# Kernel optimization log

Hardware: AMD Instinct MI355X
Metric: run time of the kernel (lower is better)

Reference implementation:

```python
import jax, jax.numpy as jnp
import numpy as np

B, T_H, N, F_P = 16, 24, 256, 6
H, PRED_LEN, F_W = 64, 12, 4


def _build_static(coords):
    # haversine distance matrix -> gaussian kernel -> threshold (epsilon=0.5)
    lon, lat = coords[:, 0], coords[:, 1]
    dlon = lon[None, :] - lon[:, None]
    dlat = lat[None, :] - lat[:, None]
    a = (np.sin(np.radians(dlat / 2)) ** 2
         + np.cos(np.radians(lat[:, None])) * np.cos(np.radians(lat[None, :]))
         * np.sin(np.radians(dlon / 2)) ** 2)
    dist = 2.0 * 6371.0 * np.arcsin(np.sqrt(np.clip(a, 0.0, None)))
    std = dist.flatten().std()
    adj = np.exp(-np.square(dist / std))
    adj[adj < 0.5] = 0.0
    return adj.astype(np.float32)


def setup_inputs() -> dict:
    key = jax.random.key(0)
    ks = jax.random.split(key, 16)
    rng = np.random.default_rng(0)
    coords_np = np.stack([116.0 + rng.uniform(-1.0, 1.0, N),
                          40.0 + rng.uniform(-1.0, 1.0, N)], axis=1).astype(np.float32)
    s = 0.05
    scale_w = jnp.asarray([1.0, 360.0, 10.0, 1.0], jnp.float32)  # [_, dir(deg), speed, _]
    return {
        "history_pollution": jax.random.normal(ks[0], (B, T_H, N, F_P), jnp.float32),
        "history_weather": jax.random.uniform(ks[1], (B, T_H, F_W), jnp.float32) * scale_w,
        "static_adj": jnp.asarray(_build_static(coords_np)),
        "coords": jnp.asarray(coords_np),
        "w_gc1": jax.random.normal(ks[2], (H, F_P), jnp.float32) * s,
        "b_gc1": jax.random.normal(ks[3], (H,), jnp.float32) * s,
        "w_gc2": jax.random.normal(ks[4], (H, H), jnp.float32) * s,
        "b_gc2": jax.random.normal(ks[5], (H,), jnp.float32) * s,
        "w_ih": jax.random.normal(ks[6], (3 * H, H), jnp.float32) * s,
        "w_hh": jax.random.normal(ks[7], (3 * H, H), jnp.float32) * s,
        "b_ih": jax.random.normal(ks[8], (3 * H,), jnp.float32) * s,
        "b_hh": jax.random.normal(ks[9], (3 * H,), jnp.float32) * s,
        "w_m1": jax.random.normal(ks[10], (32, H), jnp.float32) * s,
        "b_m1": jax.random.normal(ks[11], (32,), jnp.float32) * s,
        "w_m2": jax.random.normal(ks[12], (F_P, 32), jnp.float32) * s,
        "b_m2": jax.random.normal(ks[13], (F_P,), jnp.float32) * s,
    }


def _forward(history_pollution, history_weather, static_adj, coords,
             w_gc1, b_gc1, w_gc2, b_gc2, w_ih, w_hh, b_ih, b_hh,
             w_m1, b_m1, w_m2, b_m2):
    Bs, Th, Ns, Fp = history_pollution.shape
    dt = history_pollution.dtype
    eye = jnp.eye(Ns, dtype=dt)
    # station pair angles: vecs[i,j] = coords[j] - coords[i]
    vecs = coords[None, :, :] - coords[:, None, :]
    ang = jnp.arctan2(vecs[..., 1], vecs[..., 0])  # [N,N]

    def gconv(x, adj, w, b):
        wt = adj + eye[None]                         # [B,N,N]
        d = 1.0 / (jnp.sqrt(wt.sum(-1)) + 1e-6)      # [B,N]
        norm = d[:, :, None] * wt * d[:, None, :]    # D^-1/2 W D^-1/2
        return jnp.einsum('bij,bjf->bif', norm, x) @ w.T + b

    def gcb(x, w_out, w_in):
        h1 = jax.nn.relu(gconv(x, w_out, w_gc1, b_gc1))
        return jax.nn.relu(gconv(h1, w_in, w_gc2, b_gc2))

    def gru(h, x):                                   # h,x: [B*N,H]
        gi = x @ w_ih.T + b_ih
        gh = h @ w_hh.T + b_hh
        i_r, i_z, i_n = jnp.split(gi, 3, axis=-1)
        h_r, h_z, h_n = jnp.split(gh, 3, axis=-1)
        r = jax.nn.sigmoid(i_r + h_r)
        z = jax.nn.sigmoid(i_z + h_z)
        n = jnp.tanh(i_n + r * h_n)
        return (1.0 - z) * n + z * h

    def mlp(x):
        return jax.nn.relu(x @ w_m1.T + b_m1) @ w_m2.T + b_m2

    def enc_step(carry, xs):
        h, _ = carry
        x_t, spd, wd = xs                            # [B,N,F],[B],[B]
        rad = jnp.deg2rad(wd)
        w_dyn = jnp.maximum(spd[:, None, None] * jnp.cos(ang[None] - rad[:, None, None]), 0.0)
        w_out = static_adj[None] * w_dyn             # [B,N,N]
        sf = gcb(x_t, w_out, jnp.swapaxes(w_out, 1, 2))
        h = gru(h, sf.reshape(Bs * Ns, -1))
        return (h, w_out), None

    h0 = jnp.zeros((Bs * Ns, w_hh.shape[1]), dt)
    xs = (jnp.moveaxis(history_pollution, 1, 0),      # [T,B,N,F]
          history_weather[:, :, 2].T,                 # wind speed [T,B]
          history_weather[:, :, 1].T)                 # wind dir   [T,B]
    (h, last_w_out), _ = jax.lax.scan(enc_step, (h0, jnp.zeros((Bs, Ns, Ns), dt)), xs)
    last_w_in = jnp.swapaxes(last_w_out, 1, 2)

    dec0 = mlp(h.reshape(Bs, Ns, -1))

    def dec_step(carry, _):
        h_c, x = carry
        sf = gcb(x, last_w_out, last_w_in)
        h_c = gru(h_c, sf.reshape(Bs * Ns, -1))
        pred = mlp(h_c.reshape(Bs, Ns, -1))
        return (h_c, pred), pred

    _, preds = jax.lax.scan(dec_step, (h, dec0), None, length=PRED_LEN)
    return jnp.moveaxis(preds, 0, 1)                  # [B, pred_len, N, F_P]


def reference(history_pollution, history_weather, static_adj, coords,
              w_gc1, b_gc1, w_gc2, b_gc2, w_ih, w_hh, b_ih, b_hh,
              w_m1, b_m1, w_m2, b_m2):
    return _forward(history_pollution, history_weather, static_adj, coords,
                    w_gc1, b_gc1, w_gc2, b_gc2, w_ih, w_hh, b_ih, b_hh,
                    w_m1, b_m1, w_m2, b_m2)
```

## Files before the change

### kernel.cpp

```cpp
#include <hip/hip_runtime.h>
#include <math.h>

#define Bsz 16
#define Tt 24
#define Nn 256
#define Fp 6
#define Hh 64
#define PredL 12
#define Fw 4
#define M1 32
#define TCHUNK 12
#define DEG2RAD 0.017453292519943295f
#define IDX2(t, b) ((t) * Bsz + (b))

__global__ __launch_bounds__(256) void k_prep(
    const float* __restrict__ coords, const float* __restrict__ adj,
    const float* __restrict__ wgc2, const float* __restrict__ wih,
    const float* __restrict__ whh,  const float* __restrict__ wm1,
    const float* __restrict__ wm2,
    float2* __restrict__ pk,
    float* __restrict__ wgc2T, float* __restrict__ wm1T, float* __restrict__ wm2T,
    float4* __restrict__ wihP, float4* __restrict__ whhP) {
  int tid = threadIdx.x;
  if (blockIdx.x < Nn) {
    int i = blockIdx.x;
    int j = tid;
    float dx = coords[2 * j]     - coords[2 * i];
    float dy = coords[2 * j + 1] - coords[2 * i + 1];
    float ang = atan2f(dy, dx);
    float a = adj[i * Nn + j];
    pk[i * Nn + j] = make_float2(a * cosf(ang), a * sinf(ang));
    return;
  }
  for (int idx = tid; idx < Hh * Hh; idx += 256) {
    int g = idx / Hh, k = idx % Hh;
    wgc2T[k * Hh + g] = wgc2[g * Hh + k];
  }
  for (int idx = tid; idx < M1 * Hh; idx += 256) {
    int m = idx / Hh, k = idx % Hh;
    wm1T[k * M1 + m] = wm1[m * Hh + k];
  }
  for (int idx = tid; idx < Fp * M1; idx += 256) {
    int f = idx / M1, m = idx % M1;
    wm2T[m * Fp + f] = wm2[f * M1 + m];
  }
  for (int idx = tid; idx < Hh * 64; idx += 256) {
    int k = idx >> 6, lane = idx & 63;
    wihP[idx] = make_float4(wih[(0 * 64 + lane) * Hh + k],
                            wih[(1 * 64 + lane) * Hh + k],
                            wih[(2 * 64 + lane) * Hh + k], 0.f);
    whhP[idx] = make_float4(whh[(0 * 64 + lane) * Hh + k],
                            whh[(1 * 64 + lane) * Hh + k],
                            whh[(2 * 64 + lane) * Hh + k], 0.f);
  }
}

__global__ __launch_bounds__(256, 2) void k_enc(
    const float2* __restrict__ pk, const float* __restrict__ hp,
    const float* __restrict__ hw,
    const float* __restrict__ wgc1, const float* __restrict__ bgc1,
    const float* __restrict__ wgc2T, const float* __restrict__ bgc2,
    float* __restrict__ sf_all,
    float* __restrict__ d23, float* __restrict__ e23) {
  __shared__ float d_lds[Nn];
  __shared__ float e_lds[Nn];
  __shared__ __align__(16) float u_s[Nn * 8];
  __shared__ __align__(16) float h1_s[Nn * 68];
  int tb = blockIdx.x, t = tb / Bsz, b = tb % Bsz;
  int tid = threadIdx.x;
  float spd = hw[(b * Tt + t) * Fw + 2];
  float rad = hw[(b * Tt + t) * Fw + 1] * DEG2RAD;
  float scr = spd * cosf(rad), ssr = spd * sinf(rad);

  {
    int i = tid;
    float rs = 0.f, cs = 0.f;
#pragma unroll 4
    for (int j = 0; j < Nn; ++j) {
      float2 pv = pk[j * Nn + i];
      float v = pv.x * scr + pv.y * ssr;
      cs += fmaxf(v, 0.f);
      rs += fmaxf(-v, 0.f);
    }
    float2 pd = pk[i * Nn + i];
    float vii = pd.x * scr + pd.y * ssr;
    rs += vii;
    float di = 1.f / (sqrtf(rs + 1.f) + 1e-6f);
    float ei = 1.f / (sqrtf(cs + 1.f) + 1e-6f);
    d_lds[i] = di; e_lds[i] = ei;
    if (t == Tt - 1) { d23[b * Nn + i] = di; e23[b * Nn + i] = ei; }
  }
  __syncthreads();

  {
    const float* xsrc = hp + (long)(b * Tt + t) * Nn * Fp;
    for (int idx = tid; idx < Nn * Fp; idx += 256) {
      int j = idx / Fp, f = idx - j * Fp;
      u_s[j * 8 + f] = d_lds[j] * xsrc[idx];
    }
    u_s[tid * 8 + 6] = 0.f;
    u_s[tid * 8 + 7] = 0.f;
  }
  __syncthreads();

  {
    int i = tid;
    float a0 = 0.f, a1 = 0.f, a2 = 0.f, a3 = 0.f, a4 = 0.f, a5 = 0.f;
#pragma unroll 2
    for (int j = 0; j < Nn; ++j) {
      float2 pv = pk[j * Nn + i];
      float v = pv.x * scr + pv.y * ssr;
      float w = fmaxf(-v, 0.f);
      float4 ul = *(const float4*)&u_s[j * 8];
      float4 uh = *(const float4*)&u_s[j * 8 + 4];
      a0 += w * ul.x; a1 += w * ul.y; a2 += w * ul.z;
      a3 += w * ul.w; a4 += w * uh.x; a5 += w * uh.y;
    }
    float2 pd = pk[i * Nn + i];
    float vii = pd.x * scr + pd.y * ssr;
    float di = d_lds[i], ei = e_lds[i];
    float c1 = vii + 1.f;
    float y0 = di * (a0 + c1 * u_s[i * 8 + 0]);
    float y1 = di * (a1 + c1 * u_s[i * 8 + 1]);
    float y2 = di * (a2 + c1 * u_s[i * 8 + 2]);
    float y3 = di * (a3 + c1 * u_s[i * 8 + 3]);
    float y4 = di * (a4 + c1 * u_s[i * 8 + 4]);
    float y5 = di * (a5 + c1 * u_s[i * 8 + 5]);
#pragma unroll
    for (int g4 = 0; g4 < 16; ++g4) {
      float4 hv;
#pragma unroll
      for (int q = 0; q < 4; ++q) {
        int g = g4 * 4 + q;
        float v2 = bgc1[g] + wgc1[g * Fp + 0] * y0 + wgc1[g * Fp + 1] * y1 +
                   wgc1[g * Fp + 2] * y2 + wgc1[g * Fp + 3] * y3 +
                   wgc1[g * Fp + 4] * y4 + wgc1[g * Fp + 5] * y5;
        ((float*)&hv)[q] = fmaxf(v2, 0.f) * ei;
      }
      *(float4*)&h1_s[i * 68 + g4 * 4] = hv;
    }
  }
  __syncthreads();

  int gb = tid >> 5, rb = tid & 31;
  int i0r = rb * 8, g0 = gb * 8;
  float z[8][8];
#pragma unroll
  for (int r = 0; r < 8; ++r)
#pragma unroll
    for (int q = 0; q < 8; ++q) z[r][q] = 0.f;
#pragma unroll 2
  for (int j = 0; j < Nn; ++j) {
    float4 hA = *(const float4*)&h1_s[j * 68 + g0];
    float4 hB = *(const float4*)&h1_s[j * 68 + g0 + 4];
    const float4* pkr = (const float4*)(pk + (long)j * Nn + i0r);
    float4 p0 = pkr[0], p1 = pkr[1], p2 = pkr[2], p3 = pkr[3];
    float wv[8];
    wv[0] = fmaxf(p0.x * scr + p0.y * ssr, 0.f);
    wv[1] = fmaxf(p0.z * scr + p0.w * ssr, 0.f);
    wv[2] = fmaxf(p1.x * scr + p1.y * ssr, 0.f);
    wv[3] = fmaxf(p1.z * scr + p1.w * ssr, 0.f);
    wv[4] = fmaxf(p2.x * scr + p2.y * ssr, 0.f);
    wv[5] = fmaxf(p2.z * scr + p2.w * ssr, 0.f);
    wv[6] = fmaxf(p3.x * scr + p3.y * ssr, 0.f);
    wv[7] = fmaxf(p3.z * scr + p3.w * ssr, 0.f);
#pragma unroll
    for (int r = 0; r < 8; ++r) {
      z[r][0] += wv[r] * hA.x; z[r][1] += wv[r] * hA.y;
      z[r][2] += wv[r] * hA.z; z[r][3] += wv[r] * hA.w;
      z[r][4] += wv[r] * hB.x; z[r][5] += wv[r] * hB.y;
      z[r][6] += wv[r] * hB.z; z[r][7] += wv[r] * hB.w;
    }
  }
#pragma unroll
  for (int r = 0; r < 8; ++r) {
    int i = i0r + r;
    float4 hA = *(const float4*)&h1_s[i * 68 + g0];
    float4 hB = *(const float4*)&h1_s[i * 68 + g0 + 4];
    float ei = e_lds[i];
    z[r][0] = (z[r][0] + hA.x) * ei; z[r][1] = (z[r][1] + hA.y) * ei;
    z[r][2] = (z[r][2] + hA.z) * ei; z[r][3] = (z[r][3] + hA.w) * ei;
    z[r][4] = (z[r][4] + hB.x) * ei; z[r][5] = (z[r][5] + hB.y) * ei;
    z[r][6] = (z[r][6] + hB.z) * ei; z[r][7] = (z[r][7] + hB.w) * ei;
  }
  __syncthreads();
#pragma unroll
  for (int r = 0; r < 8; ++r) {
    *(float4*)&h1_s[(i0r + r) * 68 + g0] =
        make_float4(z[r][0], z[r][1], z[r][2], z[r][3]);
    *(float4*)&h1_s[(i0r + r) * 68 + g0 + 4] =
        make_float4(z[r][4], z[r][5], z[r][6], z[r][7]);
  }
  __syncthreads();

  {
    int i = tid;
    float4 zr[16];
#pragma unroll
    for (int k4 = 0; k4 < 16; ++k4)
      zr[k4] = *(const float4*)&h1_s[i * 68 + k4 * 4];
    long base = (long)IDX2(t, b) * Nn * Hh + (long)i * Hh;
#pragma unroll
    for (int c = 0; c < 4; ++c) {
      float s[16];
#pragma unroll
      for (int q = 0; q < 16; ++q) s[q] = bgc2[c * 16 + q];
#pragma unroll
      for (int k4 = 0; k4 < 16; ++k4) {
#pragma unroll
        for (int e = 0; e < 4; ++e) {
          int k = k4 * 4 + e;
          float zk = ((const float*)&zr[k4])[e];
#pragma unroll
          for (int q = 0; q < 16; ++q)
            s[q] += wgc2T[k * Hh + c * 16 + q] * zk;
        }
      }
#pragma unroll
      for (int q4 = 0; q4 < 4; ++q4) {
        float4 sv = make_float4(fmaxf(s[q4 * 4 + 0], 0.f), fmaxf(s[q4 * 4 + 1], 0.f),
                                fmaxf(s[q4 * 4 + 2], 0.f), fmaxf(s[q4 * 4 + 3], 0.f));
        *(float4*)&sf_all[base + c * 16 + q4 * 4] = sv;
      }
    }
  }
}

__global__ __launch_bounds__(256) void k_gi(
    const float* __restrict__ sf_all, const float4* __restrict__ wihP,
    const float* __restrict__ bih, float* __restrict__ gi, int t0) {
  __shared__ float sf_c[4][16][64];
  int tid = threadIdx.x, w = tid >> 6, lane = tid & 63;
  int rowc0 = blockIdx.x * 64 + w * 16;
  long rowg0 = (long)t0 * (Bsz * Nn) + rowc0;
#pragma unroll
  for (int rr = 0; rr < 16; ++rr)
    sf_c[w][rr][lane] = sf_all[(rowg0 + rr) * Hh + lane];
  float bi_r = bih[lane], bi_z = bih[64 + lane], bi_n = bih[128 + lane];
  float ar[16], az[16], an[16];
#pragma unroll
  for (int rr = 0; rr < 16; ++rr) { ar[rr] = bi_r; az[rr] = bi_z; an[rr] = bi_n; }
#pragma unroll 2
  for (int kb = 0; kb < 16; ++kb) {
    int k0 = kb * 4;
    float4 wi0 = wihP[(k0 + 0) * 64 + lane];
    float4 wi1 = wihP[(k0 + 1) * 64 + lane];
    float4 wi2 = wihP[(k0 + 2) * 64 + lane];
    float4 wi3 = wihP[(k0 + 3) * 64 + lane];
#pragma unroll
    for (int rr = 0; rr < 16; ++rr) {
      const float4 s4 = *(const float4*)&sf_c[w][rr][k0];
      ar[rr] += s4.x * wi0.x + s4.y * wi1.x + s4.z * wi2.x + s4.w * wi3.x;
      az[rr] += s4.x * wi0.y + s4.y * wi1.y + s4.z * wi2.y + s4.w * wi3.y;
      an[rr] += s4.x * wi0.z + s4.y * wi1.z + s4.z * wi2.z + s4.w * wi3.z;
    }
  }
#pragma unroll
  for (int rr = 0; rr < 16; ++rr) {
    long rowc = rowc0 + rr;
    gi[(rowc * 3 + 0) * 64 + lane] = ar[rr];
    gi[(rowc * 3 + 1) * 64 + lane] = az[rr];
    gi[(rowc * 3 + 2) * 64 + lane] = an[rr];
  }
}

__global__ __launch_bounds__(256) void k_gru_scan4(
    const float* __restrict__ gi, const float4* __restrict__ whhP,
    const float* __restrict__ bhh, float* __restrict__ hstate,
    int t0, int nt) {
  __shared__ float h_s[16][64];
  int b = blockIdx.x >> 4;
  int i0 = (blockIdx.x & 15) * 16;
  int tid = threadIdx.x, w = tid >> 6, lane = tid & 63;
  float bh_r = bhh[lane], bh_z = bhh[64 + lane], bh_n = bhh[128 + lane];
  float h_reg[4];
#pragma unroll
  for (int rr = 0; rr < 4; ++rr) {
    float hv = (t0 == 0) ? 0.f
                         : hstate[((long)b * Nn + i0 + w * 4 + rr) * Hh + lane];
    h_reg[rr] = hv;
    h_s[w * 4 + rr][lane] = hv;
  }
  for (int tl = 0; tl < nt; ++tl) {
    long rbase = ((long)tl * Bsz + b) * Nn + i0 + w * 4;
    float gr[4], gz[4], gn[4], hr[4], hz[4], hn[4];
#pragma unroll
    for (int rr = 0; rr < 4; ++rr) {
      gr[rr] = gi[((rbase + rr) * 3 + 0) * 64 + lane];
      gz[rr] = gi[((rbase + rr) * 3 + 1) * 64 + lane];
      gn[rr] = gi[((rbase + rr) * 3 + 2) * 64 + lane];
      hr[rr] = bh_r; hz[rr] = bh_z; hn[rr] = bh_n;
    }
#pragma unroll 4
    for (int kb = 0; kb < 16; ++kb) {
      int k0 = kb * 4;
      float4 wh0 = whhP[(k0 + 0) * 64 + lane];
      float4 wh1 = whhP[(k0 + 1) * 64 + lane];
      float4 wh2 = whhP[(k0 + 2) * 64 + lane];
      float4 wh3 = whhP[(k0 + 3) * 64 + lane];
#pragma unroll
      for (int rr = 0; rr < 4; ++rr) {
        const float4 h4 = *(const float4*)&h_s[w * 4 + rr][k0];
        hr[rr] += h4.x * wh0.x + h4.y * wh1.x + h4.z * wh2.x + h4.w * wh3.x;
        hz[rr] += h4.x * wh0.y + h4.y * wh1.y + h4.z * wh2.y + h4.w * wh3.y;
        hn[rr] += h4.x * wh0.z + h4.y * wh1.z + h4.z * wh2.z + h4.w * wh3.z;
      }
    }
#pragma unroll
    for (int rr = 0; rr < 4; ++rr) {
      float rg = 1.f / (1.f + expf(-(gr[rr] + hr[rr])));
      float zg = 1.f / (1.f + expf(-(gz[rr] + hz[rr])));
      float ng = tanhf(gn[rr] + rg * hn[rr]);
      float hv = (1.f - zg) * ng + zg * h_reg[rr];
      h_reg[rr] = hv;
      h_s[w * 4 + rr][lane] = hv;
    }
  }
#pragma unroll
  for (int rr = 0; rr < 4; ++rr)
    hstate[((long)b * Nn + i0 + w * 4 + rr) * Hh + lane] = h_reg[rr];
}

__global__ __launch_bounds__(256) void k_norm_dec(
    const float* __restrict__ hw, const float2* __restrict__ pk,
    const float* __restrict__ d23, const float* __restrict__ e23,
    float* __restrict__ A1d, float* __restrict__ A2d) {
  int b = blockIdx.x >> 8;
  int i = blockIdx.x & 255;
  int j = threadIdx.x;
  float spd = hw[(b * Tt + (Tt - 1)) * Fw + 2];
  float rad = hw[(b * Tt + (Tt - 1)) * Fw + 1] * DEG2RAD;
  float cr = cosf(rad), sr = sinf(rad);
  const float* drow = d23 + b * Nn;
  const float* erow = e23 + b * Nn;
  float2 pv = pk[i * Nn + j];
  float val = spd * (pv.x * cr + pv.y * sr);
  float dlt = (j == i) ? 1.f : 0.f;
  float wout = fmaxf(val, 0.f);
  float win  = (j == i) ? wout : fmaxf(-val, 0.f);
  A1d[((long)b * Nn + i) * Nn + j] = drow[i] * (wout + dlt) * drow[j];
  A2d[((long)b * Nn + i) * Nn + j] = erow[i] * (win + dlt) * erow[j];
}

__global__ __launch_bounds__(256) void k_dec0(
    const float* __restrict__ hstate,
    const float* __restrict__ wm1T, const float* __restrict__ bm1,
    const float* __restrict__ wm2T, const float* __restrict__ bm2,
    float* __restrict__ xnext) {
  const int RPB = 16;
  __shared__ float h_lds[RPB][Hh];
  __shared__ float u_lds[RPB][M1];
  int r0 = blockIdx.x * RPB;
  int tid = threadIdx.x;
#pragma unroll
  for (int c = 0; c < (RPB * Hh) / 256; ++c) {
    int idx = tid + c * 256;
    h_lds[idx >> 6][idx & 63] = hstate[(long)r0 * Hh + idx];
  }
  __syncthreads();
#pragma unroll
  for (int rep = 0; rep < 2; ++rep) {
    int idx = tid + rep * 256;
    int row = idx >> 5, m = idx & 31;
    float um = bm1[m];
    for (int k = 0; k < Hh; ++k) um += wm1T[k * M1 + m] * h_lds[row][k];
    u_lds[row][m] = fmaxf(um, 0.f);
  }
  __syncthreads();
  if (tid < RPB * Fp) {
    int row = tid / Fp, f = tid % Fp;
    float pf = bm2[f];
#pragma unroll
    for (int m = 0; m < M1; ++m) pf += wm2T[m * Fp + f] * u_lds[row][m];
    xnext[(r0 + row) * Fp + f] = pf;
  }
}

__global__ __launch_bounds__(256) void k_dstep_A(
    const float* __restrict__ xb, const float* __restrict__ A1d,
    const float* __restrict__ wgc1, const float* __restrict__ bgc1,
    float* __restrict__ h1d) {
  __shared__ float x_lds[Nn * Fp];
  int b = blockIdx.x >> 4;
  int i0 = (blockIdx.x & 15) * 16;
  int tid = threadIdx.x, w = tid >> 6, lane = tid & 63;
  const float* xsrc = xb + (long)b * Nn * Fp;
#pragma unroll
  for (int c = 0; c < 6; ++c) x_lds[tid + 256 * c] = xsrc[tid + 256 * c];
  __syncthreads();
#pragma unroll
  for (int rr = 0; rr < 4; ++rr) {
    int i = i0 + w * 4 + rr;
    const float* arow = A1d + ((long)b * Nn + i) * Nn;
    float acc[Fp] = {0.f, 0.f, 0.f, 0.f, 0.f, 0.f};
#pragma unroll
    for (int c = 0; c < 4; ++c) {
      int j = lane + 64 * c;
      float wt = arow[j];
#pragma unroll
      for (int f = 0; f < Fp; ++f) acc[f] += wt * x_lds[j * Fp + f];
    }
#pragma unroll
    for (int f = 0; f < Fp; ++f) {
#pragma unroll
      for (int off = 32; off; off >>= 1) acc[f] += __shfl_xor(acc[f], off);
    }
    float hv = bgc1[lane];
#pragma unroll
    for (int f = 0; f < Fp; ++f) hv += wgc1[lane * Fp + f] * acc[f];
    h1d[((long)b * Nn + i) * Hh + lane] = fmaxf(hv, 0.f);
  }
}

__global__ __launch_bounds__(256) void k_dstep_B(
    const float* __restrict__ A2d, const float* __restrict__ h1d,
    const float* __restrict__ wgc2T, const float* __restrict__ bgc2,
    const float4* __restrict__ wihP, const float4* __restrict__ whhP,
    const float* __restrict__ bih, const float* __restrict__ bhh,
    float* __restrict__ hstate,
    const float* __restrict__ wm1T, const float* __restrict__ bm1,
    const float* __restrict__ wm2T, const float* __restrict__ bm2,
    float* __restrict__ outp, float* __restrict__ xnext, int p) {
  __shared__ __align__(16) float wvT[Nn * 20];
  __shared__ float red[4][16][Hh];
  __shared__ float y2[16][Hh];
  __shared__ float sf_s[16][Hh];
  __shared__ float h_s[16][Hh];
  __shared__ float hn_lds[16][Hh];
  __shared__ float u_lds[16][M1];
  int b = blockIdx.x >> 4;
  int i0 = (blockIdx.x & 15) * 16;
  int tid = threadIdx.x, w = tid >> 6, lane = tid & 63;

#pragma unroll
  for (int r = 0; r < 16; ++r)
    wvT[tid * 20 + r] = A2d[((long)b * Nn + i0 + r) * Nn + tid];
  float hp_reg[4];
#pragma unroll
  for (int rr = 0; rr < 4; ++rr) {
    hp_reg[rr] = hstate[((long)b * Nn + i0 + w * 4 + rr) * Hh + lane];
    h_s[w * 4 + rr][lane] = hp_reg[rr];
  }
  __syncthreads();

  float acc[16];
#pragma unroll
  for (int r = 0; r < 16; ++r) acc[r] = 0.f;
  const float* h1b = h1d + (long)b * Nn * Hh;
#pragma unroll 4
  for (int jj = 0; jj < 64; ++jj) {
    int j = w * 64 + jj;
    float hv = h1b[j * Hh + lane];
    const float4* wp = (const float4*)(wvT + j * 20);
    float4 w0 = wp[0], w1 = wp[1], w2 = wp[2], w3 = wp[3];
    acc[0] += w0.x * hv; acc[1] += w0.y * hv; acc[2] += w0.z * hv; acc[3] += w0.w * hv;
    acc[4] += w1.x * hv; acc[5] += w1.y * hv; acc[6] += w1.z * hv; acc[7] += w1.w * hv;
    acc[8] += w2.x * hv; acc[9] += w2.y * hv; acc[10] += w2.z * hv; acc[11] += w2.w * hv;
    acc[12] += w3.x * hv; acc[13] += w3.y * hv; acc[14] += w3.z * hv; acc[15] += w3.w * hv;
  }
#pragma unroll
  for (int r = 0; r < 16; ++r) red[w][r][lane] = acc[r];
  __syncthreads();
#pragma unroll
  for (int rr = 0; rr < 4; ++rr) {
    int r = w * 4 + rr;
    y2[r][lane] = red[0][r][lane] + red[1][r][lane] + red[2][r][lane] + red[3][r][lane];
  }
  {
    float a0 = bgc2[lane], a1 = a0, a2 = a0, a3 = a0;
    for (int k = 0; k < Hh; ++k) {
      float wk = wgc2T[k * Hh + lane];
      a0 += wk * y2[w * 4 + 0][k];
      a1 += wk * y2[w * 4 + 1][k];
      a2 += wk * y2[w * 4 + 2][k];
      a3 += wk * y2[w * 4 + 3][k];
    }
    sf_s[w * 4 + 0][lane] = fmaxf(a0, 0.f);
    sf_s[w * 4 + 1][lane] = fmaxf(a1, 0.f);
    sf_s[w * 4 + 2][lane] = fmaxf(a2, 0.f);
    sf_s[w * 4 + 3][lane] = fmaxf(a3, 0.f);
  }

  float hn_reg[4];
  {
    float bi_r = bih[lane], bi_z = bih[64 + lane], bi_n = bih[128 + lane];
    float bh_r = bhh[lane], bh_z = bhh[64 + lane], bh_n = bhh[128 + lane];
    float gir[4], giz[4], gin[4], ghr[4], ghz[4], ghn[4];
#pragma unroll
    for (int rr = 0; rr < 4; ++rr) {
      gir[rr] = bi_r; giz[rr] = bi_z; gin[rr] = bi_n;
      ghr[rr] = bh_r; ghz[rr] = bh_z; ghn[rr] = bh_n;
    }
#pragma unroll 4
    for (int kb = 0; kb < 16; ++kb) {
      int k0 = kb * 4;
      float4 wi[4], wh[4];
#pragma unroll
      for (int q = 0; q < 4; ++q) {
        wi[q] = wihP[(k0 + q) * 64 + lane];
        wh[q] = whhP[(k0 + q) * 64 + lane];
      }
#pragma unroll
      for (int rr = 0; rr < 4; ++rr) {
        const float4 s4 = *(const float4*)&sf_s[w * 4 + rr][k0];
        const float4 h4 = *(const float4*)&h_s[w * 4 + rr][k0];
        gir[rr] += s4.x * wi[0].x + s4.y * wi[1].x + s4.z * wi[2].x + s4.w * wi[3].x;
        giz[rr] += s4.x * wi[0].y + s4.y * wi[1].y + s4.z * wi[2].y + s4.w * wi[3].y;
        gin[rr] += s4.x * wi[0].z + s4.y * wi[1].z + s4.z * wi[2].z + s4.w * wi[3].z;
        ghr[rr] += h4.x * wh[0].x + h4.y * wh[1].x + h4.z * wh[2].x + h4.w * wh[3].x;
        ghz[rr] += h4.x * wh[0].y + h4.y * wh[1].y + h4.z * wh[2].y + h4.w * wh[3].y;
        ghn[rr] += h4.x * wh[0].z + h4.y * wh[1].z + h4.z * wh[2].z + h4.w * wh[3].z;
      }
    }
#pragma unroll
    for (int rr = 0; rr < 4; ++rr) {
      float rg = 1.f / (1.f + expf(-(gir[rr] + ghr[rr])));
      float zg = 1.f / (1.f + expf(-(giz[rr] + ghz[rr])));
      float ng = tanhf(gin[rr] + rg * ghn[rr]);
      hn_reg[rr] = (1.f - zg) * ng + zg * hp_reg[rr];
      hstate[((long)b * Nn + i0 + w * 4 + rr) * Hh + lane] = hn_reg[rr];
      hn_lds[w * 4 + rr][lane] = hn_reg[rr];
    }
  }
  __syncthreads();
#pragma unroll
  for (int rep = 0; rep < 2; ++rep) {
    int idx = tid + rep * 256;
    int row = idx >> 5, m = idx & 31;
    float um = bm1[m];
    for (int k = 0; k < Hh; ++k) um += wm1T[k * M1 + m] * hn_lds[row][k];
    u_lds[row][m] = fmaxf(um, 0.f);
  }
  __syncthreads();
  if (tid < 16 * Fp) {
    int row = tid / Fp, f = tid % Fp;
    float pf = bm2[f];
#pragma unroll
    for (int m = 0; m < M1; ++m) pf += wm2T[m * Fp + f] * u_lds[row][m];
    int i = i0 + row;
    outp[(((long)b * PredL + p) * Nn + i) * Fp + f] = pf;
    xnext[((long)b * Nn + i) * Fp + f] = pf;
  }
}

extern "C" void kernel_launch(void* const* d_in, const int* in_sizes, int n_in,
                              void* d_out, int out_size, void* d_ws, size_t ws_size,
                              hipStream_t stream) {
  const float* hp     = (const float*)d_in[0];
  const float* hw     = (const float*)d_in[1];
  const float* adj    = (const float*)d_in[2];
  const float* coords = (const float*)d_in[3];
  const float* wgc1   = (const float*)d_in[4];
  const float* bgc1   = (const float*)d_in[5];
  const float* wgc2   = (const float*)d_in[6];
  const float* bgc2   = (const float*)d_in[7];
  const float* wih    = (const float*)d_in[8];
  const float* whh    = (const float*)d_in[9];
  const float* bih    = (const float*)d_in[10];
  const float* bhh    = (const float*)d_in[11];
  const float* wm1    = (const float*)d_in[12];
  const float* bm1    = (const float*)d_in[13];
  const float* wm2    = (const float*)d_in[14];
  const float* bm2    = (const float*)d_in[15];
  float* out = (float*)d_out;

  float* w = (float*)d_ws;
  float2* pk    = (float2*)w; w += Nn * Nn * 2;
  float* d23    = w; w += Bsz * Nn;
  float* e23    = w; w += Bsz * Nn;
  float* hstate = w; w += Bsz * Nn * Hh;
  float* sf_all = w; w += (long)Tt * Bsz * Nn * Hh;
  float* gi_ch  = w; w += (long)TCHUNK * Bsz * Nn * 3 * 64;
  float* h1d    = w; w += Bsz * Nn * Hh;
  float* xb0    = w; w += Bsz * Nn * Fp;
  float* xb1    = w; w += Bsz * Nn * Fp;
  float* A1d    = w; w += Bsz * Nn * Nn;
  float* A2d    = w; w += Bsz * Nn * Nn;
  float* wgc2T  = w; w += Hh * Hh;
  float* wm1T   = w; w += Hh * M1;
  float* wm2T   = w; w += M1 * Fp;
  float4* wihP  = (float4*)w; w += Hh * 64 * 4;
  float4* whhP  = (float4*)w; w += Hh * 64 * 4;

  k_prep<<<Nn + 1, 256, 0, stream>>>(coords, adj, wgc2, wih, whh, wm1, wm2,
                                     pk, wgc2T, wm1T, wm2T, wihP, whhP);
  k_enc<<<Tt * Bsz, 256, 0, stream>>>(pk, hp, hw, wgc1, bgc1, wgc2T, bgc2,
                                      sf_all, d23, e23);
  for (int s = 0; s < Tt / TCHUNK; ++s) {
    int t0 = s * TCHUNK;
    k_gi<<<(TCHUNK * Bsz * Nn) / 64, 256, 0, stream>>>(sf_all, wihP, bih,
                                                       gi_ch, t0);
    k_gru_scan4<<<Bsz * 16, 256, 0, stream>>>(gi_ch, whhP, bhh, hstate,
                                              t0, TCHUNK);
  }
  k_norm_dec<<<Bsz * Nn, 256, 0, stream>>>(hw, pk, d23, e23, A1d, A2d);
  k_dec0<<<Bsz * Nn / 16, 256, 0, stream>>>(hstate, wm1T, bm1, wm2T, bm2, xb0);

  for (int p = 0; p < PredL; ++p) {
    float* xin  = (p & 1) ? xb1 : xb0;
    float* xout = (p & 1) ? xb0 : xb1;
    k_dstep_A<<<Bsz * 16, 256, 0, stream>>>(xin, A1d, wgc1, bgc1, h1d);
    k_dstep_B<<<Bsz * 16, 256, 0, stream>>>(
        A2d, h1d, wgc2T, bgc2, wihP, whhP, bih, bhh, hstate,
        wm1T, bm1, wm2T, bm2, out, xout, p);
  }
}
```

Baseline: 762.6 us.

## Fuse decoder step kernels and merge norm/dec0 setup, restructure encoder second GCN

Decoder step A and B are fused into one kernel per step. Each block recomputes the full first graph-conv layer (A1^T x, then wgc1) in LDS and then handles 32 rows, which removes the h1d round trip and one launch per step. The normalized-adjacency and dec0 kernels are merged into a single launch. In the encoder, the second graph conv is changed to one thread per node with 64 accumulators, and launch_bounds min-blocks is dropped. The cost is redundant first-layer work in every block, fewer blocks (128) in the decoder, and higher register pressure in the encoder.

```diff
diff --git a/kernel.cpp b/kernel.cpp
--- a/kernel.cpp
+++ b/kernel.cpp
@@ -55,7 +55,7 @@
   }
 }
 
-__global__ __launch_bounds__(256, 2) void k_enc(
+__global__ __launch_bounds__(256) void k_enc(
     const float2* __restrict__ pk, const float* __restrict__ hp,
     const float* __restrict__ hw,
     const float* __restrict__ wgc1, const float* __restrict__ bgc1,
@@ -68,12 +68,12 @@
   __shared__ __align__(16) float h1_s[Nn * 68];
   int tb = blockIdx.x, t = tb / Bsz, b = tb % Bsz;
   int tid = threadIdx.x;
+  int i = tid;
   float spd = hw[(b * Tt + t) * Fw + 2];
   float rad = hw[(b * Tt + t) * Fw + 1] * DEG2RAD;
   float scr = spd * cosf(rad), ssr = spd * sinf(rad);
 
   {
-    int i = tid;
     float rs = 0.f, cs = 0.f;
 #pragma unroll 4
     for (int j = 0; j < Nn; ++j) {
@@ -104,7 +104,6 @@
   __syncthreads();
 
   {
-    int i = tid;
     float a0 = 0.f, a1 = 0.f, a2 = 0.f, a3 = 0.f, a4 = 0.f, a5 = 0.f;
 #pragma unroll 2
     for (int j = 0; j < Nn; ++j) {
@@ -142,87 +141,53 @@
   }
   __syncthreads();
 
-  int gb = tid >> 5, rb = tid & 31;
-  int i0r = rb * 8, g0 = gb * 8;
-  float z[8][8];
-#pragma unroll
-  for (int r = 0; r < 8; ++r)
-#pragma unroll
-    for (int q = 0; q < 8; ++q) z[r][q] = 0.f;
+  float z[64];
+#pragma unroll
+  for (int k = 0; k < 64; ++k) z[k] = 0.f;
 #pragma unroll 2
   for (int j = 0; j < Nn; ++j) {
-    float4 hA = *(const float4*)&h1_s[j * 68 + g0];
-    float4 hB = *(const float4*)&h1_s[j * 68 + g0 + 4];
-    const float4* pkr = (const float4*)(pk + (long)j * Nn + i0r);
-    float4 p0 = pkr[0], p1 = pkr[1], p2 = pkr[2], p3 = pkr[3];
-    float wv[8];
-    wv[0] = fmaxf(p0.x * scr + p0.y * ssr, 0.f);
-    wv[1] = fmaxf(p0.z * scr + p0.w * ssr, 0.f);
-    wv[2] = fmaxf(p1.x * scr + p1.y * ssr, 0.f);
-    wv[3] = fmaxf(p1.z * scr + p1.w * ssr, 0.f);
-    wv[4] = fmaxf(p2.x * scr + p2.y * ssr, 0.f);
-    wv[5] = fmaxf(p2.z * scr + p2.w * ssr, 0.f);
-    wv[6] = fmaxf(p3.x * scr + p3.y * ssr, 0.f);
-    wv[7] = fmaxf(p3.z * scr + p3.w * ssr, 0.f);
-#pragma unroll
-    for (int r = 0; r < 8; ++r) {
-      z[r][0] += wv[r] * hA.x; z[r][1] += wv[r] * hA.y;
-      z[r][2] += wv[r] * hA.z; z[r][3] += wv[r] * hA.w;
-      z[r][4] += wv[r] * hB.x; z[r][5] += wv[r] * hB.y;
-      z[r][6] += wv[r] * hB.z; z[r][7] += wv[r] * hB.w;
-    }
-  }
-#pragma unroll
-  for (int r = 0; r < 8; ++r) {
-    int i = i0r + r;
-    float4 hA = *(const float4*)&h1_s[i * 68 + g0];
-    float4 hB = *(const float4*)&h1_s[i * 68 + g0 + 4];
+    float2 pv = pk[j * Nn + i];
+    float v = pv.x * scr + pv.y * ssr;
+    float wf = fmaxf(v, 0.f) + ((j == i) ? 1.f : 0.f);
+#pragma unroll
+    for (int g4 = 0; g4 < 16; ++g4) {
+      float4 h4 = *(const float4*)&h1_s[j * 68 + g4 * 4];
+      z[g4 * 4 + 0] += wf * h4.x;
+      z[g4 * 4 + 1] += wf * h4.y;
+      z[g4 * 4 + 2] += wf * h4.z;
+      z[g4 * 4 + 3] += wf * h4.w;
+    }
+  }
+  {
     float ei = e_lds[i];
-    z[r][0] = (z[r][0] + hA.x) * ei; z[r][1] = (z[r][1] + hA.y) * ei;
-    z[r][2] = (z[r][2] + hA.z) * ei; z[r][3] = (z[r][3] + hA.w) * ei;
-    z[r][4] = (z[r][4] + hB.x) * ei; z[r][5] = (z[r][5] + hB.y) * ei;
-    z[r][6] = (z[r][6] + hB.z) * ei; z[r][7] = (z[r][7] + hB.w) * ei;
-  }
-  __syncthreads();
-#pragma unroll
-  for (int r = 0; r < 8; ++r) {
-    *(float4*)&h1_s[(i0r + r) * 68 + g0] =
-        make_float4(z[r][0], z[r][1], z[r][2], z[r][3]);
-    *(float4*)&h1_s[(i0r + r) * 68 + g0 + 4] =
-        make_float4(z[r][4], z[r][5], z[r][6], z[r][7]);
-  }
-  __syncthreads();
-
-  {
-    int i = tid;
-    float4 zr[16];
-#pragma unroll
-    for (int k4 = 0; k4 < 16; ++k4)
-      zr[k4] = *(const float4*)&h1_s[i * 68 + k4 * 4];
-    long base = (long)IDX2(t, b) * Nn * Hh + (long)i * Hh;
-#pragma unroll
-    for (int c = 0; c < 4; ++c) {
-      float s[16];
-#pragma unroll
-      for (int q = 0; q < 16; ++q) s[q] = bgc2[c * 16 + q];
-#pragma unroll
-      for (int k4 = 0; k4 < 16; ++k4) {
-#pragma unroll
-        for (int e = 0; e < 4; ++e) {
-          int k = k4 * 4 + e;
-          float zk = ((const float*)&zr[k4])[e];
-#pragma unroll
-          for (int q = 0; q < 16; ++q)
-            s[q] += wgc2T[k * Hh + c * 16 + q] * zk;
-        }
-      }
-#pragma unroll
-      for (int q4 = 0; q4 < 4; ++q4) {
-        float4 sv = make_float4(fmaxf(s[q4 * 4 + 0], 0.f), fmaxf(s[q4 * 4 + 1], 0.f),
-                                fmaxf(s[q4 * 4 + 2], 0.f), fmaxf(s[q4 * 4 + 3], 0.f));
-        *(float4*)&sf_all[base + c * 16 + q4 * 4] = sv;
-      }
-    }
+#pragma unroll
+    for (int k = 0; k < 64; ++k) z[k] *= ei;
+  }
+  __syncthreads();
+
+#pragma unroll
+  for (int c = 0; c < 4; ++c) {
+    float s[16];
+#pragma unroll
+    for (int q = 0; q < 16; ++q) s[q] = bgc2[c * 16 + q];
+#pragma unroll
+    for (int k = 0; k < 64; ++k) {
+      float zk = z[k];
+#pragma unroll
+      for (int q = 0; q < 16; ++q) s[q] += wgc2T[k * Hh + c * 16 + q] * zk;
+    }
+#pragma unroll
+    for (int q4 = 0; q4 < 4; ++q4) {
+      float4 sv = make_float4(fmaxf(s[q4 * 4 + 0], 0.f), fmaxf(s[q4 * 4 + 1], 0.f),
+                              fmaxf(s[q4 * 4 + 2], 0.f), fmaxf(s[q4 * 4 + 3], 0.f));
+      *(float4*)&h1_s[i * 68 + c * 16 + q4 * 4] = sv;
+    }
+  }
+  __syncthreads();
+  long base = (long)IDX2(t, b) * Nn * Hh;
+  for (int idx = tid; idx < Nn * 16; idx += 256) {
+    int j = idx >> 4, g4 = idx & 15;
+    *(float4*)&sf_all[base + j * Hh + g4 * 4] = *(const float4*)&h1_s[j * 68 + g4 * 4];
   }
 }
 
@@ -321,39 +286,37 @@
     hstate[((long)b * Nn + i0 + w * 4 + rr) * Hh + lane] = h_reg[rr];
 }
 
-__global__ __launch_bounds__(256) void k_norm_dec(
+__global__ __launch_bounds__(256) void k_misc(
     const float* __restrict__ hw, const float2* __restrict__ pk,
     const float* __restrict__ d23, const float* __restrict__ e23,
-    float* __restrict__ A1d, float* __restrict__ A2d) {
-  int b = blockIdx.x >> 8;
-  int i = blockIdx.x & 255;
-  int j = threadIdx.x;
-  float spd = hw[(b * Tt + (Tt - 1)) * Fw + 2];
-  float rad = hw[(b * Tt + (Tt - 1)) * Fw + 1] * DEG2RAD;
-  float cr = cosf(rad), sr = sinf(rad);
-  const float* drow = d23 + b * Nn;
-  const float* erow = e23 + b * Nn;
-  float2 pv = pk[i * Nn + j];
-  float val = spd * (pv.x * cr + pv.y * sr);
-  float dlt = (j == i) ? 1.f : 0.f;
-  float wout = fmaxf(val, 0.f);
-  float win  = (j == i) ? wout : fmaxf(-val, 0.f);
-  A1d[((long)b * Nn + i) * Nn + j] = drow[i] * (wout + dlt) * drow[j];
-  A2d[((long)b * Nn + i) * Nn + j] = erow[i] * (win + dlt) * erow[j];
-}
-
-__global__ __launch_bounds__(256) void k_dec0(
+    float* __restrict__ AT, float* __restrict__ A2d,
     const float* __restrict__ hstate,
     const float* __restrict__ wm1T, const float* __restrict__ bm1,
     const float* __restrict__ wm2T, const float* __restrict__ bm2,
     float* __restrict__ xnext) {
-  const int RPB = 16;
-  __shared__ float h_lds[RPB][Hh];
-  __shared__ float u_lds[RPB][M1];
-  int r0 = blockIdx.x * RPB;
+  __shared__ float h_lds[16][Hh];
+  __shared__ float u_lds[16][M1];
   int tid = threadIdx.x;
-#pragma unroll
-  for (int c = 0; c < (RPB * Hh) / 256; ++c) {
+  if (blockIdx.x < Bsz * Nn) {
+    int b = blockIdx.x >> 8;
+    int i = blockIdx.x & 255;
+    int j = tid;
+    float spd = hw[(b * Tt + (Tt - 1)) * Fw + 2];
+    float rad = hw[(b * Tt + (Tt - 1)) * Fw + 1] * DEG2RAD;
+    float cr = cosf(rad), sr = sinf(rad);
+    const float* drow = d23 + b * Nn;
+    const float* erow = e23 + b * Nn;
+    float2 pv = pk[i * Nn + j];
+    float val = spd * (pv.x * cr + pv.y * sr);
+    float dlt = (j == i) ? 1.f : 0.f;
+    float wtji = (j == i) ? fmaxf(val, 0.f) : fmaxf(-val, 0.f);
+    AT[((long)b * Nn + i) * Nn + j]  = drow[j] * (wtji + dlt) * drow[i];
+    A2d[((long)b * Nn + i) * Nn + j] = erow[i] * (wtji + dlt) * erow[j];
+    return;
+  }
+  int r0 = (blockIdx.x - Bsz * Nn) * 16;
+#pragma unroll
+  for (int c = 0; c < 4; ++c) {
     int idx = tid + c * 256;
     h_lds[idx >> 6][idx & 63] = hstate[(long)r0 * Hh + idx];
   }
@@ -367,7 +330,7 @@
     u_lds[row][m] = fmaxf(um, 0.f);
   }
   __syncthreads();
-  if (tid < RPB * Fp) {
+  if (tid < 16 * Fp) {
     int row = tid / Fp, f = tid % Fp;
     float pf = bm2[f];
 #pragma unroll
@@ -376,122 +339,115 @@
   }
 }
 
-__global__ __launch_bounds__(256) void k_dstep_A(
-    const float* __restrict__ xb, const float* __restrict__ A1d,
-    const float* __restrict__ wgc1, const float* __restrict__ bgc1,
-    float* __restrict__ h1d) {
-  __shared__ float x_lds[Nn * Fp];
-  int b = blockIdx.x >> 4;
-  int i0 = (blockIdx.x & 15) * 16;
-  int tid = threadIdx.x, w = tid >> 6, lane = tid & 63;
-  const float* xsrc = xb + (long)b * Nn * Fp;
-#pragma unroll
-  for (int c = 0; c < 6; ++c) x_lds[tid + 256 * c] = xsrc[tid + 256 * c];
-  __syncthreads();
-#pragma unroll
-  for (int rr = 0; rr < 4; ++rr) {
-    int i = i0 + w * 4 + rr;
-    const float* arow = A1d + ((long)b * Nn + i) * Nn;
-    float acc[Fp] = {0.f, 0.f, 0.f, 0.f, 0.f, 0.f};
-#pragma unroll
-    for (int c = 0; c < 4; ++c) {
-      int j = lane + 64 * c;
-      float wt = arow[j];
-#pragma unroll
-      for (int f = 0; f < Fp; ++f) acc[f] += wt * x_lds[j * Fp + f];
-    }
-#pragma unroll
-    for (int f = 0; f < Fp; ++f) {
-#pragma unroll
-      for (int off = 32; off; off >>= 1) acc[f] += __shfl_xor(acc[f], off);
-    }
-    float hv = bgc1[lane];
-#pragma unroll
-    for (int f = 0; f < Fp; ++f) hv += wgc1[lane * Fp + f] * acc[f];
-    h1d[((long)b * Nn + i) * Hh + lane] = fmaxf(hv, 0.f);
-  }
-}
-
-__global__ __launch_bounds__(256) void k_dstep_B(
-    const float* __restrict__ A2d, const float* __restrict__ h1d,
-    const float* __restrict__ wgc2T, const float* __restrict__ bgc2,
+__global__ __launch_bounds__(256) void k_dstep(
+    const float* __restrict__ AT, const float* __restrict__ A2d,
+    const float* __restrict__ xb_in, float* __restrict__ hstate,
     const float4* __restrict__ wihP, const float4* __restrict__ whhP,
+    const float* __restrict__ wgc2T, const float* __restrict__ wgc1,
+    const float* __restrict__ bgc1, const float* __restrict__ bgc2,
     const float* __restrict__ bih, const float* __restrict__ bhh,
-    float* __restrict__ hstate,
     const float* __restrict__ wm1T, const float* __restrict__ bm1,
     const float* __restrict__ wm2T, const float* __restrict__ bm2,
-    float* __restrict__ outp, float* __restrict__ xnext, int p) {
-  __shared__ __align__(16) float wvT[Nn * 20];
-  __shared__ float red[4][16][Hh];
-  __shared__ float y2[16][Hh];
-  __shared__ float sf_s[16][Hh];
-  __shared__ float h_s[16][Hh];
-  __shared__ float hn_lds[16][Hh];
-  __shared__ float u_lds[16][M1];
-  int b = blockIdx.x >> 4;
-  int i0 = (blockIdx.x & 15) * 16;
-  int tid = threadIdx.x, w = tid >> 6, lane = tid & 63;
-
-#pragma unroll
-  for (int r = 0; r < 16; ++r)
-    wvT[tid * 20 + r] = A2d[((long)b * Nn + i0 + r) * Nn + tid];
-  float hp_reg[4];
-#pragma unroll
-  for (int rr = 0; rr < 4; ++rr) {
-    hp_reg[rr] = hstate[((long)b * Nn + i0 + w * 4 + rr) * Hh + lane];
-    h_s[w * 4 + rr][lane] = hp_reg[rr];
-  }
-  __syncthreads();
-
-  float acc[16];
-#pragma unroll
-  for (int r = 0; r < 16; ++r) acc[r] = 0.f;
-  const float* h1b = h1d + (long)b * Nn * Hh;
+    float* __restrict__ outp, float* __restrict__ xb_out, int p) {
+  __shared__ __align__(16) float x_s[Nn * 8];
+  __shared__ __align__(16) float y_s[Nn * 8];
+  __shared__ float h1_s[Nn * Hh];
+  __shared__ float z_s[32][Hh];
+  __shared__ float sf_s[32][Hh];
+  __shared__ float hp_s[32][Hh];
+  __shared__ float u_s2[32][M1];
+
+  int b = blockIdx.x >> 3;
+  int i0 = (blockIdx.x & 7) * 32;
+  int tid = threadIdx.x;
+  int lane = tid & 63;
+  int wu = __builtin_amdgcn_readfirstlane(tid >> 6);
+
+  for (int idx = tid; idx < Nn * Fp; idx += 256) {
+    int j = idx / Fp, f = idx - j * Fp;
+    x_s[j * 8 + f] = xb_in[(long)b * Nn * Fp + idx];
+  }
+  x_s[tid * 8 + 6] = 0.f;
+  x_s[tid * 8 + 7] = 0.f;
+#pragma unroll
+  for (int c = 0; c < 8; ++c) {
+    int idx = tid + c * 256;
+    hp_s[idx >> 6][idx & 63] = hstate[((long)b * Nn + i0) * Hh + idx];
+  }
+  __syncthreads();
+
+  {
+    float a0 = 0.f, a1 = 0.f, a2 = 0.f, a3 = 0.f, a4 = 0.f, a5 = 0.f;
+    const float* atb = AT + (long)b * Nn * Nn;
 #pragma unroll 4
-  for (int jj = 0; jj < 64; ++jj) {
-    int j = w * 64 + jj;
-    float hv = h1b[j * Hh + lane];
-    const float4* wp = (const float4*)(wvT + j * 20);
-    float4 w0 = wp[0], w1 = wp[1], w2 = wp[2], w3 = wp[3];
-    acc[0] += w0.x * hv; acc[1] += w0.y * hv; acc[2] += w0.z * hv; acc[3] += w0.w * hv;
-    acc[4] += w1.x * hv; acc[5] += w1.y * hv; acc[6] += w1.z * hv; acc[7] += w1.w * hv;
-    acc[8] += w2.x * hv; acc[9] += w2.y * hv; acc[10] += w2.z * hv; acc[11] += w2.w * hv;
-    acc[12] += w3.x * hv; acc[13] += w3.y * hv; acc[14] += w3.z * hv; acc[15] += w3.w * hv;
-  }
-#pragma unroll
-  for (int r = 0; r < 16; ++r) red[w][r][lane] = acc[r];
-  __syncthreads();
-#pragma unroll
-  for (int rr = 0; rr < 4; ++rr) {
-    int r = w * 4 + rr;
-    y2[r][lane] = red[0][r][lane] + red[1][r][lane] + red[2][r][lane] + red[3][r][lane];
-  }
-  {
-    float a0 = bgc2[lane], a1 = a0, a2 = a0, a3 = a0;
+    for (int m = 0; m < Nn; ++m) {
+      float av = atb[m * Nn + tid];
+      float4 xl = *(const float4*)&x_s[m * 8];
+      float4 xh = *(const float4*)&x_s[m * 8 + 4];
+      a0 += av * xl.x; a1 += av * xl.y; a2 += av * xl.z;
+      a3 += av * xl.w; a4 += av * xh.x; a5 += av * xh.y;
+    }
+    y_s[tid * 8 + 0] = a0; y_s[tid * 8 + 1] = a1; y_s[tid * 8 + 2] = a2;
+    y_s[tid * 8 + 3] = a3; y_s[tid * 8 + 4] = a4; y_s[tid * 8 + 5] = a5;
+  }
+  __syncthreads();
+
+  {
+    float wg0 = wgc1[lane * Fp + 0], wg1 = wgc1[lane * Fp + 1];
+    float wg2 = wgc1[lane * Fp + 2], wg3 = wgc1[lane * Fp + 3];
+    float wg4 = wgc1[lane * Fp + 4], wg5 = wgc1[lane * Fp + 5];
+    float bg = bgc1[lane];
+#pragma unroll 4
+    for (int jj = 0; jj < 64; ++jj) {
+      int j = wu * 64 + jj;
+      float4 yl = *(const float4*)&y_s[j * 8];
+      float4 yh = *(const float4*)&y_s[j * 8 + 4];
+      float hv = bg + wg0 * yl.x + wg1 * yl.y + wg2 * yl.z + wg3 * yl.w +
+                 wg4 * yh.x + wg5 * yh.y;
+      h1_s[j * Hh + lane] = fmaxf(hv, 0.f);
+    }
+  }
+  __syncthreads();
+
+  {
+    float acc[8];
+#pragma unroll
+    for (int q = 0; q < 8; ++q) acc[q] = 0.f;
+    const float* a2 = A2d + ((long)b * Nn + i0 + wu * 8) * Nn;
+#pragma unroll 2
+    for (int j = 0; j < Nn; ++j) {
+      float hv = h1_s[j * Hh + lane];
+#pragma unroll
+      for (int q = 0; q < 8; ++q) acc[q] += a2[q * Nn + j] * hv;
+    }
+#pragma unroll
+    for (int q = 0; q < 8; ++q) z_s[wu * 8 + q][lane] = acc[q];
+  }
+
+  {
+    float s[8];
+    float bv = bgc2[lane];
+#pragma unroll
+    for (int q = 0; q < 8; ++q) s[q] = bv;
     for (int k = 0; k < Hh; ++k) {
       float wk = wgc2T[k * Hh + lane];
-      a0 += wk * y2[w * 4 + 0][k];
-      a1 += wk * y2[w * 4 + 1][k];
-      a2 += wk * y2[w * 4 + 2][k];
-      a3 += wk * y2[w * 4 + 3][k];
-    }
-    sf_s[w * 4 + 0][lane] = fmaxf(a0, 0.f);
-    sf_s[w * 4 + 1][lane] = fmaxf(a1, 0.f);
-    sf_s[w * 4 + 2][lane] = fmaxf(a2, 0.f);
-    sf_s[w * 4 + 3][lane] = fmaxf(a3, 0.f);
-  }
-
-  float hn_reg[4];
+#pragma unroll
+      for (int q = 0; q < 8; ++q) s[q] += wk * z_s[wu * 8 + q][k];
+    }
+#pragma unroll
+    for (int q = 0; q < 8; ++q) sf_s[wu * 8 + q][lane] = fmaxf(s[q], 0.f);
+  }
+
   {
     float bi_r = bih[lane], bi_z = bih[64 + lane], bi_n = bih[128 + lane];
     float bh_r = bhh[lane], bh_z = bhh[64 + lane], bh_n = bhh[128 + lane];
-    float gir[4], giz[4], gin[4], ghr[4], ghz[4], ghn[4];
-#pragma unroll
-    for (int rr = 0; rr < 4; ++rr) {
-      gir[rr] = bi_r; giz[rr] = bi_z; gin[rr] = bi_n;
-      ghr[rr] = bh_r; ghz[rr] = bh_z; ghn[rr] = bh_n;
-    }
-#pragma unroll 4
+    float gir[8], giz[8], gin[8], ghr[8], ghz[8], ghn[8];
+#pragma unroll
+    for (int q = 0; q < 8; ++q) {
+      gir[q] = bi_r; giz[q] = bi_z; gin[q] = bi_n;
+      ghr[q] = bh_r; ghz[q] = bh_z; ghn[q] = bh_n;
+    }
+#pragma unroll 2
     for (int kb = 0; kb < 16; ++kb) {
       int k0 = kb * 4;
       float4 wi[4], wh[4];
@@ -501,45 +457,46 @@
         wh[q] = whhP[(k0 + q) * 64 + lane];
       }
 #pragma unroll
-      for (int rr = 0; rr < 4; ++rr) {
-        const float4 s4 = *(const float4*)&sf_s[w * 4 + rr][k0];
-        const float4 h4 = *(const float4*)&h_s[w * 4 + rr][k0];
-        gir[rr] += s4.x * wi[0].x + s4.y * wi[1].x + s4.z * wi[2].x + s4.w * wi[3].x;
-        giz[rr] += s4.x * wi[0].y + s4.y * wi[1].y + s4.z * wi[2].y + s4.w * wi[3].y;
-        gin[rr] += s4.x * wi[0].z + s4.y * wi[1].z + s4.z * wi[2].z + s4.w * wi[3].z;
-        ghr[rr] += h4.x * wh[0].x + h4.y * wh[1].x + h4.z * wh[2].x + h4.w * wh[3].x;
-        ghz[rr] += h4.x * wh[0].y + h4.y * wh[1].y + h4.z * wh[2].y + h4.w * wh[3].y;
-        ghn[rr] += h4.x * wh[0].z + h4.y * wh[1].z + h4.z * wh[2].z + h4.w * wh[3].z;
+      for (int q = 0; q < 8; ++q) {
+        const float4 s4 = *(const float4*)&sf_s[wu * 8 + q][k0];
+        const float4 h4 = *(const float4*)&hp_s[wu * 8 + q][k0];
+        gir[q] += s4.x * wi[0].x + s4.y * wi[1].x + s4.z * wi[2].x + s4.w * wi[3].x;
+        giz[q] += s4.x * wi[0].y + s4.y * wi[1].y + s4.z * wi[2].y + s4.w * wi[3].y;
+        gin[q] += s4.x * wi[0].z + s4.y * wi[1].z + s4.z * wi[2].z + s4.w * wi[3].z;
+        ghr[q] += h4.x * wh[0].x + h4.y * wh[1].x + h4.z * wh[2].x + h4.w * wh[3].x;
+        ghz[q] += h4.x * wh[0].y + h4.y * wh[1].y + h4.z * wh[2].y + h4.w * wh[3].y;
+        ghn[q] += h4.x * wh[0].z + h4.y * wh[1].z + h4.z * wh[2].z + h4.w * wh[3].z;
       }
     }
 #pragma unroll
-    for (int rr = 0; rr < 4; ++rr) {
-      float rg = 1.f / (1.f + expf(-(gir[rr] + ghr[rr])));
-      float zg = 1.f / (1.f + expf(-(giz[rr] + ghz[rr])));
-      float ng = tanhf(gin[rr] + rg * ghn[rr]);
-      hn_reg[rr] = (1.f - zg) * ng + zg * hp_reg[rr];
-      hstate[((long)b * Nn + i0 + w * 4 + rr) * Hh + lane] = hn_reg[rr];
-      hn_lds[w * 4 + rr][lane] = hn_reg[rr];
-    }
-  }
-  __syncthreads();
-#pragma unroll
-  for (int rep = 0; rep < 2; ++rep) {
-    int idx = tid + rep * 256;
+    for (int q = 0; q < 8; ++q) {
+      float rg = 1.f / (1.f + expf(-(gir[q] + ghr[q])));
+      float zg = 1.f / (1.f + expf(-(giz[q] + ghz[q])));
+      float ng = tanhf(gin[q] + rg * ghn[q]);
+      float hn = (1.f - zg) * ng + zg * hp_s[wu * 8 + q][lane];
+      hstate[((long)b * Nn + i0 + wu * 8 + q) * Hh + lane] = hn;
+      z_s[wu * 8 + q][lane] = hn;
+    }
+  }
+  __syncthreads();
+
+#pragma unroll
+  for (int c = 0; c < 4; ++c) {
+    int idx = tid + c * 256;
     int row = idx >> 5, m = idx & 31;
     float um = bm1[m];
-    for (int k = 0; k < Hh; ++k) um += wm1T[k * M1 + m] * hn_lds[row][k];
-    u_lds[row][m] = fmaxf(um, 0.f);
-  }
-  __syncthreads();
-  if (tid < 16 * Fp) {
-    int row = tid / Fp, f = tid % Fp;
+    for (int k = 0; k < Hh; ++k) um += wm1T[k * M1 + m] * z_s[row][k];
+    u_s2[row][m] = fmaxf(um, 0.f);
+  }
+  __syncthreads();
+  if (tid < 32 * Fp) {
+    int row = tid / Fp, f = tid - row * Fp;
     float pf = bm2[f];
 #pragma unroll
-    for (int m = 0; m < M1; ++m) pf += wm2T[m * Fp + f] * u_lds[row][m];
+    for (int m = 0; m < M1; ++m) pf += wm2T[m * Fp + f] * u_s2[row][m];
     int i = i0 + row;
     outp[(((long)b * PredL + p) * Nn + i) * Fp + f] = pf;
-    xnext[((long)b * Nn + i) * Fp + f] = pf;
+    xb_out[((long)b * Nn + i) * Fp + f] = pf;
   }
 }
 
@@ -571,10 +528,9 @@
   float* hstate = w; w += Bsz * Nn * Hh;
   float* sf_all = w; w += (long)Tt * Bsz * Nn * Hh;
   float* gi_ch  = w; w += (long)TCHUNK * Bsz * Nn * 3 * 64;
-  float* h1d    = w; w += Bsz * Nn * Hh;
   float* xb0    = w; w += Bsz * Nn * Fp;
   float* xb1    = w; w += Bsz * Nn * Fp;
-  float* A1d    = w; w += Bsz * Nn * Nn;
+  float* AT     = w; w += Bsz * Nn * Nn;
   float* A2d    = w; w += Bsz * Nn * Nn;
   float* wgc2T  = w; w += Hh * Hh;
   float* wm1T   = w; w += Hh * M1;
@@ -593,15 +549,14 @@
     k_gru_scan4<<<Bsz * 16, 256, 0, stream>>>(gi_ch, whhP, bhh, hstate,
                                               t0, TCHUNK);
   }
-  k_norm_dec<<<Bsz * Nn, 256, 0, stream>>>(hw, pk, d23, e23, A1d, A2d);
-  k_dec0<<<Bsz * Nn / 16, 256, 0, stream>>>(hstate, wm1T, bm1, wm2T, bm2, xb0);
+  k_misc<<<Bsz * Nn + Bsz * Nn / 16, 256, 0, stream>>>(
+      hw, pk, d23, e23, AT, A2d, hstate, wm1T, bm1, wm2T, bm2, xb0);
 
   for (int p = 0; p < PredL; ++p) {
     float* xin  = (p & 1) ? xb1 : xb0;
     float* xout = (p & 1) ? xb0 : xb1;
-    k_dstep_A<<<Bsz * 16, 256, 0, stream>>>(xin, A1d, wgc1, bgc1, h1d);
-    k_dstep_B<<<Bsz * 16, 256, 0, stream>>>(
-        A2d, h1d, wgc2T, bgc2, wihP, whhP, bih, bhh, hstate,
-        wm1T, bm1, wm2T, bm2, out, xout, p);
-  }
-}
+    k_dstep<<<Bsz * 8, 256, 0, stream>>>(
+        AT, A2d, xin, hstate, wihP, whhP, wgc2T, wgc1, bgc1, bgc2,
+        bih, bhh, wm1T, bm1, wm2T, bm2, out, xout, p);
+  }
+}
```

After: 1.165 ms. +52.8%, slower.
